# Kernel optimization log

Hardware: AMD Instinct MI355X
Metric: run time of the kernel (lower is better)

The kernel has to match this reference:

```python
import jax, jax.numpy as jnp
import numpy as np


def setup_inputs() -> dict:
    key = jax.random.key(0)
    k1, k2 = jax.random.split(key)
    B, V = 1024, 128000
    logits = jax.random.normal(k1, (B, V), dtype=jnp.float32)
    labels = jax.random.randint(k2, (B,), 0, V, dtype=jnp.int64)
    return {"logits": logits, "labels": labels}


def reference(logits, labels):
    # Vocab-parallel cross-entropy collapsed to single-device math:
    # global max across all splits, exp, global exp-sum, softmax,
    # gather label probability, -log, mean over batch.
    m = jnp.max(logits, axis=1, keepdims=True)            # [B, 1] global max
    exp_logit = jnp.exp(logits - m)                       # [B, V]
    exp_sum_all = jnp.sum(exp_logit, axis=1, keepdims=True)  # [B, 1] reduce_add
    softmax = exp_logit / exp_sum_all                     # [B, V]
    B = logits.shape[0]
    label_prob = softmax[jnp.arange(B), labels]           # sparse one-hot gather
    loss = jnp.mean(-jnp.log(label_prob))
    return loss
```

## Files before the change

kernel.cpp:

```cpp
#include <hip/hip_runtime.h>
#include <math.h>


#define VOCAB 128000
#define BATCH 1024
#define SPLITS 5
#define TPB 256
#define CHUNK4 (VOCAB / 4 / SPLITS)

__global__ __launch_bounds__(TPB) void ce_partial_kernel(const float* __restrict__ logits,
                                                         float* __restrict__ part_m,
                                                         float* __restrict__ part_s) {
    const int blk = blockIdx.x;
    const int row = blk / SPLITS;
    const int split = blk % SPLITS;
    const float4* __restrict__ rp =
        reinterpret_cast<const float4*>(logits + (size_t)row * VOCAB) + split * CHUNK4;

    float m = -INFINITY;
    float s = 0.0f;

    #pragma unroll 5
    for (int i = threadIdx.x; i < CHUNK4; i += TPB) {
        float4 v = rp[i];
        float m4 = fmaxf(fmaxf(v.x, v.y), fmaxf(v.z, v.w));
        float mn = fmaxf(m, m4);
        s = s * __expf(m - mn)
            + __expf(v.x - mn) + __expf(v.y - mn)
            + __expf(v.z - mn) + __expf(v.w - mn);
        m = mn;
    }

    #pragma unroll
    for (int off = 1; off < 64; off <<= 1) {
        float mo = __shfl_down(m, off);
        float so = __shfl_down(s, off);
        float mn = fmaxf(m, mo);
        s = s * __expf(m - mn) + so * __expf(mo - mn);
        m = mn;
    }

    __shared__ float sm[TPB / 64], ss[TPB / 64];
    const int wave = threadIdx.x >> 6;
    if ((threadIdx.x & 63) == 0) { sm[wave] = m; ss[wave] = s; }
    __syncthreads();

    if (threadIdx.x == 0) {
        float M = sm[0], S = ss[0];
        #pragma unroll
        for (int w = 1; w < TPB / 64; ++w) {
            float mn = fmaxf(M, sm[w]);
            S = S * __expf(M - mn) + ss[w] * __expf(sm[w] - mn);
            M = mn;
        }
        part_m[blk] = M;
        part_s[blk] = S;
    }
}

__global__ __launch_bounds__(TPB) void ce_combine_kernel(const float* __restrict__ part_m,
                                                         const float* __restrict__ part_s,
                                                         const float* __restrict__ logits,
                                                         const int* __restrict__ labels,
                                                         float* __restrict__ out) {
    float local = 0.0f;
    for (int r = threadIdx.x; r < BATCH; r += TPB) {
        float M = part_m[r * SPLITS];
        float S = part_s[r * SPLITS];
        #pragma unroll
        for (int k = 1; k < SPLITS; ++k) {
            float pm = part_m[r * SPLITS + k];
            float ps = part_s[r * SPLITS + k];
            float mn = fmaxf(M, pm);
            S = S * __expf(M - mn) + ps * __expf(pm - mn);
            M = mn;
        }
        float xl = logits[(size_t)r * VOCAB + labels[r]];
        local += (M - xl) + __logf(S);
    }

    #pragma unroll
    for (int off = 1; off < 64; off <<= 1) local += __shfl_down(local, off);

    __shared__ float sv[TPB / 64];
    if ((threadIdx.x & 63) == 0) sv[threadIdx.x >> 6] = local;
    __syncthreads();
    if (threadIdx.x == 0) {
        float t = 0.0f;
        #pragma unroll
        for (int w = 0; w < TPB / 64; ++w) t += sv[w];
        out[0] = t / (float)BATCH;
    }
}

extern "C" void kernel_launch(void* const* d_in, const int* in_sizes, int n_in,
                              void* d_out, int out_size, void* d_ws, size_t ws_size,
                              hipStream_t stream) {
    const float* logits = (const float*)d_in[0];
    const int* labels = (const int*)d_in[1];
    float* part_m = (float*)d_ws;
    float* part_s = (float*)d_ws + BATCH * SPLITS;
    float* out = (float*)d_out;

    ce_partial_kernel<<<BATCH * SPLITS, TPB, 0, stream>>>(logits, part_m, part_s);
    ce_combine_kernel<<<1, TPB, 0, stream>>>(part_m, part_s, logits, labels, out);
}
```

Baseline: 98.14 us.

## Split rows across more blocks with one-shot loads and move label gather into partials

The vocab split goes from 5 to 25, so each thread issues exactly five nontemporal float4 loads up front. It then does a two-pass max and exp-sum in registers instead of the loop-carried online softmax rescale. The block that owns the label gathers the label logit, and the combine kernel uses 1024 threads with one row each. The aim is more memory parallelism, shorter dependency chains, and a shorter serial combine tail, at the cost of five times more partial results and more blocks.

```diff
diff --git a/kernel.cpp b/kernel.cpp
--- a/kernel.cpp
+++ b/kernel.cpp
@@ -4,37 +4,50 @@
 
 #define VOCAB 128000
 #define BATCH 1024
-#define SPLITS 5
+#define SPLITS 25
 #define TPB 256
-#define CHUNK4 (VOCAB / 4 / SPLITS)
+#define CHUNK (VOCAB / SPLITS)
+#define CHUNK4 (CHUNK / 4)
+
+typedef float f32x4 __attribute__((ext_vector_type(4)));
 
 __global__ __launch_bounds__(TPB) void ce_partial_kernel(const float* __restrict__ logits,
+                                                         const int* __restrict__ labels,
                                                          float* __restrict__ part_m,
-                                                         float* __restrict__ part_s) {
+                                                         float* __restrict__ part_s,
+                                                         float* __restrict__ row_xl) {
     const int blk = blockIdx.x;
     const int row = blk / SPLITS;
     const int split = blk % SPLITS;
-    const float4* __restrict__ rp =
-        reinterpret_cast<const float4*>(logits + (size_t)row * VOCAB) + split * CHUNK4;
+    const float* rowp = logits + (size_t)row * VOCAB;
+    const f32x4* __restrict__ rp =
+        reinterpret_cast<const f32x4*>(rowp + split * CHUNK);
 
-    float m = -INFINITY;
-    float s = 0.0f;
+    const int t = threadIdx.x;
+    f32x4 v0 = __builtin_nontemporal_load(rp + t);
+    f32x4 v1 = __builtin_nontemporal_load(rp + t + TPB);
+    f32x4 v2 = __builtin_nontemporal_load(rp + t + 2 * TPB);
+    f32x4 v3 = __builtin_nontemporal_load(rp + t + 3 * TPB);
+    f32x4 v4 = __builtin_nontemporal_load(rp + t + 4 * TPB);
 
-    #pragma unroll 5
-    for (int i = threadIdx.x; i < CHUNK4; i += TPB) {
-        float4 v = rp[i];
-        float m4 = fmaxf(fmaxf(v.x, v.y), fmaxf(v.z, v.w));
-        float mn = fmaxf(m, m4);
-        s = s * __expf(m - mn)
-            + __expf(v.x - mn) + __expf(v.y - mn)
-            + __expf(v.z - mn) + __expf(v.w - mn);
-        m = mn;
-    }
+    float m0 = fmaxf(fmaxf(v0[0], v0[1]), fmaxf(v0[2], v0[3]));
+    float m1 = fmaxf(fmaxf(v1[0], v1[1]), fmaxf(v1[2], v1[3]));
+    float m2 = fmaxf(fmaxf(v2[0], v2[1]), fmaxf(v2[2], v2[3]));
+    float m3 = fmaxf(fmaxf(v3[0], v3[1]), fmaxf(v3[2], v3[3]));
+    float m4 = fmaxf(fmaxf(v4[0], v4[1]), fmaxf(v4[2], v4[3]));
+    float m = fmaxf(fmaxf(fmaxf(m0, m1), fmaxf(m2, m3)), m4);
+
+    float s0 = __expf(v0[0] - m) + __expf(v0[1] - m) + __expf(v0[2] - m) + __expf(v0[3] - m);
+    float s1 = __expf(v1[0] - m) + __expf(v1[1] - m) + __expf(v1[2] - m) + __expf(v1[3] - m);
+    float s2 = __expf(v2[0] - m) + __expf(v2[1] - m) + __expf(v2[2] - m) + __expf(v2[3] - m);
+    float s3 = __expf(v3[0] - m) + __expf(v3[1] - m) + __expf(v3[2] - m) + __expf(v3[3] - m);
+    float s4 = __expf(v4[0] - m) + __expf(v4[1] - m) + __expf(v4[2] - m) + __expf(v4[3] - m);
+    float s = ((s0 + s1) + (s2 + s3)) + s4;
 
     #pragma unroll
     for (int off = 1; off < 64; off <<= 1) {
-        float mo = __shfl_down(m, off);
-        float so = __shfl_down(s, off);
+        float mo = __shfl_xor(m, off);
+        float so = __shfl_xor(s, off);
         float mn = fmaxf(m, mo);
         s = s * __expf(m - mn) + so * __expf(mo - mn);
         m = mn;
@@ -55,40 +68,41 @@
         }
         part_m[blk] = M;
         part_s[blk] = S;
+
+        int lab = labels[row];
+        int lo = split * CHUNK;
+        if (lab >= lo && lab < lo + CHUNK) row_xl[row] = rowp[lab];
     }
 }
 
-__global__ __launch_bounds__(TPB) void ce_combine_kernel(const float* __restrict__ part_m,
-                                                         const float* __restrict__ part_s,
-                                                         const float* __restrict__ logits,
-                                                         const int* __restrict__ labels,
-                                                         float* __restrict__ out) {
-    float local = 0.0f;
-    for (int r = threadIdx.x; r < BATCH; r += TPB) {
-        float M = part_m[r * SPLITS];
-        float S = part_s[r * SPLITS];
-        #pragma unroll
-        for (int k = 1; k < SPLITS; ++k) {
-            float pm = part_m[r * SPLITS + k];
-            float ps = part_s[r * SPLITS + k];
-            float mn = fmaxf(M, pm);
-            S = S * __expf(M - mn) + ps * __expf(pm - mn);
-            M = mn;
-        }
-        float xl = logits[(size_t)r * VOCAB + labels[r]];
-        local += (M - xl) + __logf(S);
+#define CTPB 1024
+__global__ __launch_bounds__(CTPB) void ce_combine_kernel(const float* __restrict__ part_m,
+                                                          const float* __restrict__ part_s,
+                                                          const float* __restrict__ row_xl,
+                                                          float* __restrict__ out) {
+    const int r = threadIdx.x;
+    float M = part_m[r * SPLITS];
+    float S = part_s[r * SPLITS];
+    #pragma unroll
+    for (int k = 1; k < SPLITS; ++k) {
+        float pm = part_m[r * SPLITS + k];
+        float ps = part_s[r * SPLITS + k];
+        float mn = fmaxf(M, pm);
+        S = S * __expf(M - mn) + ps * __expf(pm - mn);
+        M = mn;
     }
+    float loss = (M - row_xl[r]) + __logf(S);
 
     #pragma unroll
-    for (int off = 1; off < 64; off <<= 1) local += __shfl_down(local, off);
+    for (int off = 1; off < 64; off <<= 1) loss += __shfl_xor(loss, off);
 
-    __shared__ float sv[TPB / 64];
-    if ((threadIdx.x & 63) == 0) sv[threadIdx.x >> 6] = local;
+    __shared__ float sv[CTPB / 64];
+    if ((threadIdx.x & 63) == 0) sv[threadIdx.x >> 6] = loss;
     __syncthreads();
     if (threadIdx.x == 0) {
         float t = 0.0f;
         #pragma unroll
-        for (int w = 0; w < TPB / 64; ++w) t += sv[w];
+        for (int w = 0; w < CTPB / 64; ++w) t += sv[w];
         out[0] = t / (float)BATCH;
     }
 }
@@ -99,9 +113,11 @@
     const float* logits = (const float*)d_in[0];
     const int* labels = (const int*)d_in[1];
     float* part_m = (float*)d_ws;
-    float* part_s = (float*)d_ws + BATCH * SPLITS;
+    float* part_s = part_m + BATCH * SPLITS;
+    float* row_xl = part_s + BATCH * SPLITS;
     float* out = (float*)d_out;
 
-    ce_partial_kernel<<<BATCH * SPLITS, TPB, 0, stream>>>(logits, part_m, part_s);
-    ce_combine_kernel<<<1, TPB, 0, stream>>>(part_m, part_s, logits, labels, out);
+    ce_partial_kernel<<<BATCH * SPLITS, TPB, 0, stream>>>(logits, labels,
+                                                          part_m, part_s, row_xl);
+    ce_combine_kernel<<<1, CTPB, 0, stream>>>(part_m, part_s, row_xl, out);
 }
```

New measurement: 86.53 us. 1.13x faster.
